# Optimization experiments

Hardware: AMD Instinct MI355X
Metric: run time of the kernel (lower is better)

Reference implementation:

```python
import jax, jax.numpy as jnp
import numpy as np

V, D, H, L, FF, NA, NB, S, C, BS = 32000, 768, 12, 6, 3072, 2, 2, 512, 10, 16
MOE_LAYERS = (1, 3, 5)
NE = NA * NB


def _ln(x, g, b, eps=1e-5):
    m = x.mean(-1, keepdims=True)
    v = ((x - m) ** 2).mean(-1, keepdims=True)
    return (x - m) / jnp.sqrt(v + eps) * g + b


def _ffn(x, W1, B1, W2, B2):
    # GLU-style FFN: w2(a * silu(b)) where [a, b] = chunk(w1(x), 2)
    h = x @ W1.T + B1
    a, b = jnp.split(h, 2, -1)
    return (a * jax.nn.silu(b)) @ W2.T + B2


def _mha(x, wqkv, bqkv, wo, bo):
    Bq, Sq, d = x.shape
    dh = d // H
    qkv = x @ wqkv.T + bqkv
    q, k, v = jnp.split(qkv, 3, -1)
    q = q.reshape(Bq, Sq, H, dh).transpose(0, 2, 1, 3)
    k = k.reshape(Bq, Sq, H, dh).transpose(0, 2, 1, 3)
    v = v.reshape(Bq, Sq, H, dh).transpose(0, 2, 1, 3)
    scores = jnp.einsum('bhqd,bhkd->bhqk', q, k) / jnp.sqrt(jnp.float32(dh))
    attn = jax.nn.softmax(scores, axis=-1)
    o = jnp.einsum('bhqk,bhkd->bhqd', attn, v)
    o = o.transpose(0, 2, 1, 3).reshape(Bq, Sq, d)
    return o @ wo.T + bo


def _moe(xf, W1, B1, W2, B2, gAw, gAb, gBw, gBb):
    pA = jax.nn.softmax(xf @ gAw.T + gAb, axis=-1)  # [T, NA]
    pB = jax.nn.softmax(xf @ gBw.T + gBb, axis=-1)  # [T, NB]
    iA = jnp.argmax(pA, -1)
    iB = jnp.argmax(pB, -1)
    auxA = NA * (pA.mean(0) * jax.nn.one_hot(iA, NA).mean(0)).sum()
    auxB = NB * (pB.mean(0) * jax.nn.one_hot(iB, NB).mean(0)).sum()
    e = iA * NB + iB  # [T] flattened expert id
    # dense all-expert compute then per-token select (E is small = 4)
    h = jnp.einsum('td,efd->etf', xf, W1) + B1[:, None, :]  # [NE, T, 2*FF]
    a, b = jnp.split(h, 2, -1)
    y = jnp.einsum('etf,edf->etd', a * jax.nn.silu(b), W2) + B2[:, None, :]
    out = y[e, jnp.arange(xf.shape[0])]  # [T, D]
    return out, auxA + auxB


def _forward(tok_emb, pos_emb, wqkv, bqkv, wo, bo, ln1g, ln1b, ln2g, ln2b,
             dW1, dB1, dW2, dB2, mW1, mB1, mW2, mB2, gAw, gAb, gBw, gBb,
             cW1, cB1, cW2, cB2, input_ids):
    x = tok_emb[input_ids] + pos_emb[None, :, :]
    total_aux = jnp.float32(0.0)
    di = mi = 0
    for l in range(L):
        x = _ln(x + _mha(x, wqkv[l], bqkv[l], wo[l], bo[l]), ln1g[l], ln1b[l])
        if l in MOE_LAYERS:
            xf = x.reshape(BS * S, D)
            f, aux = _moe(xf, mW1[mi], mB1[mi], mW2[mi], mB2[mi],
                          gAw[mi], gAb[mi], gBw[mi], gBb[mi])
            mi += 1
            total_aux = total_aux + aux
            f = f.reshape(BS, S, D)
        else:
            f = _ffn(x, dW1[di], dB1[di], dW2[di], dB2[di])
            di += 1
        x = _ln(x + f, ln2g[l], ln2b[l])
    rep = x.mean(1)  # mean pooling (no cls token / mask)
    hcls = jax.nn.relu(rep @ cW1.T + cB1)
    logits = hcls @ cW2.T + cB2
    return logits, total_aux


def setup_inputs() -> dict:
    key = jax.random.key(0)
    ks = iter(jax.random.split(key, 48))
    r = lambda shape, s=0.02: jax.random.normal(next(ks), shape, jnp.float32) * s
    Ld, Lm = L - len(MOE_LAYERS), len(MOE_LAYERS)
    return dict(
        input_ids=jax.random.randint(next(ks), (BS, S), 0, V),
        tok_emb=r((V, D)),
        pos_emb=r((S, D), 0.01),
        wqkv=r((L, 3 * D, D)), bqkv=jnp.zeros((L, 3 * D), jnp.float32),
        wo=r((L, D, D)), bo=jnp.zeros((L, D), jnp.float32),
        ln1g=jnp.ones((L, D), jnp.float32), ln1b=jnp.zeros((L, D), jnp.float32),
        ln2g=jnp.ones((L, D), jnp.float32), ln2b=jnp.zeros((L, D), jnp.float32),
        dW1=r((Ld, 2 * FF, D)), dB1=jnp.zeros((Ld, 2 * FF), jnp.float32),
        dW2=r((Ld, D, FF)), dB2=jnp.zeros((Ld, D), jnp.float32),
        mW1=r((Lm, NE, 2 * FF, D)), mB1=jnp.zeros((Lm, NE, 2 * FF), jnp.float32),
        mW2=r((Lm, NE, D, FF)), mB2=jnp.zeros((Lm, NE, D), jnp.float32),
        gAw=r((Lm, NA, D)), gAb=jnp.zeros((Lm, NA), jnp.float32),
        gBw=r((Lm, NB, D)), gBb=jnp.zeros((Lm, NB), jnp.float32),
        cW1=r((D, D)), cB1=jnp.zeros((D,), jnp.float32),
        cW2=r((C, D)), cB2=jnp.zeros((C,), jnp.float32),
    )


def reference(input_ids, tok_emb, pos_emb, wqkv, bqkv, wo, bo, ln1g, ln1b,
              ln2g, ln2b, dW1, dB1, dW2, dB2, mW1, mB1, mW2, mB2,
              gAw, gAb, gBw, gBb, cW1, cB1, cW2, cB2):
    return _forward(tok_emb, pos_emb, wqkv, bqkv, wo, bo, ln1g, ln1b, ln2g,
                    ln2b, dW1, dB1, dW2, dB2, mW1, mB1, mW2, mB2,
                    gAw, gAb, gBw, gBb, cW1, cB1, cW2, cB2, input_ids)
```

## Files before the change

kernel.cpp:

```cpp
#include <hip/hip_runtime.h>
#include <cstddef>

#define TOK   8192
#define DIMD  768
#define NH    12
#define DHD   64
#define SEQ   512
#define NB_   16
#define FFD   3072
#define NEXP  4
#define CCLS  10
#define FF2   (2*FFD)

typedef short bf16x8 __attribute__((ext_vector_type(8)));
typedef float f32x4  __attribute__((ext_vector_type(4)));

static const size_t OFF_X    = 0;
static const size_t OFF_XB   = OFF_X   + (size_t)TOK*DIMD;
static const size_t OFF_F    = OFF_XB  + (size_t)TOK*DIMD/2;
static const size_t OFF_SH   = OFF_F   + (size_t)TOK*DIMD;
static const size_t SH_FL    = (size_t)8704*FF2/2;
static const size_t OFF_WQ   = OFF_SH  + SH_FL;
static const size_t OFF_WOB  = OFF_WQ  + (size_t)3*DIMD*DIMD/2;
static const size_t OFF_W1B  = OFF_WOB + (size_t)DIMD*DIMD/2;
static const size_t OFF_W2B  = OFF_W1B + (size_t)NEXP*FF2*DIMD/2;
static const size_t OFF_REP  = OFF_W2B + (size_t)NEXP*DIMD*FFD/2;
static const size_t OFF_HCLS = OFF_REP + (size_t)NB_*DIMD;
static const size_t OFF_STAT = OFF_HCLS+ (size_t)NB_*DIMD;
static const size_t OFF_INT  = OFF_STAT+ 8;
static const size_t OFF_AUX  = OFF_INT + 160;
static const size_t OFF_EID  = OFF_AUX + 1;
static const size_t OFF_PERM = OFF_EID + TOK;

__device__ __forceinline__ ushort f2bf(float f) {
    union { float f; unsigned u; } v; v.f = f;
    unsigned r = v.u + 0x7FFF + ((v.u >> 16) & 1);
    return (ushort)(r >> 16);
}
__device__ __forceinline__ float bf2f(ushort u) {
    union { unsigned u; float f; } v; v.u = ((unsigned)u) << 16;
    return v.f;
}
__device__ __forceinline__ void gload16(const void* g, void* l) {
    __builtin_amdgcn_global_load_lds((const __attribute__((address_space(1))) void*)g,
                                     (__attribute__((address_space(3))) void*)l, 16, 0, 0);
}

__global__ __launch_bounds__(256) void k_cvt(const float* __restrict__ s, ushort* __restrict__ d, int n8)
{
    int i = blockIdx.x * 256 + threadIdx.x;
    if (i >= n8) return;
    float4 x0 = ((const float4*)s)[i * 2];
    float4 x1 = ((const float4*)s)[i * 2 + 1];
    ushort r[8] = { f2bf(x0.x), f2bf(x0.y), f2bf(x0.z), f2bf(x0.w),
                    f2bf(x1.x), f2bf(x1.y), f2bf(x1.z), f2bf(x1.w) };
    ((uint4*)d)[i] = *(uint4*)r;
}

__global__ __launch_bounds__(256) void k_embed(const int* __restrict__ ids,
                                               const float* __restrict__ te,
                                               const float* __restrict__ pe,
                                               float* __restrict__ x,
                                               ushort* __restrict__ xb)
{
    int i = blockIdx.x * 256 + threadIdx.x;
    const int nd4 = DIMD / 4;
    if (i >= TOK * nd4) return;
    int t = i / nd4, d4 = i % nd4;
    int s = t % SEQ;
    int id = ids[t];
    float4 a = ((const float4*)(te + (size_t)id * DIMD))[d4];
    float4 b = ((const float4*)(pe + (size_t)s  * DIMD))[d4];
    float4 o; o.x = a.x + b.x; o.y = a.y + b.y; o.z = a.z + b.z; o.w = a.w + b.w;
    ((float4*)(x + (size_t)t * DIMD))[d4] = o;
    ushort4 ob = make_ushort4(f2bf(o.x), f2bf(o.y), f2bf(o.z), f2bf(o.w));
    *(ushort4*)(xb + (size_t)t * DIMD + d4 * 4) = ob;
}

template<int GATHER, int SCAT>
__global__ __launch_bounds__(256) void k_mm(const ushort* __restrict__ A,
                                            const ushort* __restrict__ Wb,
                                            const float* __restrict__ bias,
                                            ushort* __restrict__ C_,
                                            int N, int K, int lda,
                                            const int* __restrict__ perm,
                                            const int* __restrict__ offs,
                                            const int* __restrict__ blke,
                                            const int* __restrict__ blkb,
                                            const int* __restrict__ nblk)
{
    constexpr int MOE = GATHER || SCAT;
    __shared__ ushort As[2][4096];
    __shared__ ushort Bs[2][4096];
    __shared__ int    toks[128];
    const int tid = threadIdx.x, lane = tid & 63, w = tid >> 6;
    int bid = blockIdx.y * gridDim.x + blockIdx.x;
    int nwg = gridDim.x * gridDim.y;
    int q = nwg >> 3, r8 = nwg & 7;
    int xcd = bid & 7, loc = bid >> 3;
    int lbid = (xcd < r8 ? xcd * (q + 1) : r8 * (q + 1) + (xcd - r8) * q) + loc;
    const int bx = lbid % gridDim.x, by = lbid / gridDim.x;
    const int n0 = bx * 128, row0 = by * 128;
    const ushort* W = Wb;
    const float*  bi = bias;
    int lb = 0, cnt = 1 << 30;
    if constexpr (MOE) {
        if (by >= *nblk) return;
        int e = blke[by];
        lb = blkb[by];
        int base = offs[e];
        cnt = offs[e + 1] - base;
        W  += (size_t)e * N * K;
        bi += (size_t)e * N;
        if (tid < 128) { int rg = lb + tid; toks[tid] = perm[base + (rg < cnt ? rg : cnt - 1)]; }
        __syncthreads();
    }
    int ar0, ar1;
    if constexpr (GATHER) { ar0 = toks[lane]; ar1 = toks[64 + lane]; }
    else                  { ar0 = row0 + lane; ar1 = row0 + 64 + lane; }
    const ushort* ap0 = A + (size_t)ar0 * lda + w * 8;
    const ushort* ap1 = A + (size_t)ar1 * lda + w * 8;
    const ushort* bp0 = W + (size_t)(n0 + lane) * K + w * 8;
    const ushort* bp1 = W + (size_t)(n0 + 64 + lane) * K + w * 8;

    const int l15 = lane & 15, l4 = lane >> 4;
    const int wm = w >> 1, wn = w & 1;
    f32x4 acc[4][4] = {};

    gload16(ap0, &As[0][w * 1024]);
    gload16(ap1, &As[0][w * 1024 + 512]);
    gload16(bp0, &Bs[0][w * 1024]);
    gload16(bp1, &Bs[0][w * 1024 + 512]);
    __syncthreads();

    const int NT = K / 32;
    int cur = 0;
    for (int t = 0; t < NT; ++t) {
        if (t + 1 < NT) {
            int ko = (t + 1) * 32;
            gload16(ap0 + ko, &As[cur ^ 1][w * 1024]);
            gload16(ap1 + ko, &As[cur ^ 1][w * 1024 + 512]);
            gload16(bp0 + ko, &Bs[cur ^ 1][w * 1024]);
            gload16(bp1 + ko, &Bs[cur ^ 1][w * 1024 + 512]);
        }
        bf16x8 af[4], bf_[4];
#pragma unroll
        for (int i = 0; i < 4; ++i) {
            af[i]  = *(const bf16x8*)&As[cur][l4 * 1024 + (wm * 64 + i * 16 + l15) * 8];
            bf_[i] = *(const bf16x8*)&Bs[cur][l4 * 1024 + (wn * 64 + i * 16 + l15) * 8];
        }
#pragma unroll
        for (int mi = 0; mi < 4; ++mi)
#pragma unroll
            for (int ni = 0; ni < 4; ++ni)
                acc[mi][ni] = __builtin_amdgcn_mfma_f32_16x16x32_bf16(af[mi], bf_[ni], acc[mi][ni], 0, 0, 0);
        __syncthreads();
        cur ^= 1;
    }
#pragma unroll
    for (int ni = 0; ni < 4; ++ni) {
        int col = n0 + wn * 64 + ni * 16 + l15;
        float bb = bi[col];
#pragma unroll
        for (int mi = 0; mi < 4; ++mi) {
            int ri = wm * 64 + mi * 16 + l4 * 4;
#pragma unroll
            for (int r = 0; r < 4; ++r) {
                float o = acc[mi][ni][r] + bb;
                if constexpr (SCAT) {
                    if (lb + ri + r < cnt)
                        C_[(size_t)toks[ri + r] * N + col] = f2bf(o);
                } else {
                    C_[(size_t)(row0 + ri + r) * N + col] = f2bf(o);
                }
            }
        }
    }
}

template<int MOE>
__global__ __launch_bounds__(256) void k_w1g(const ushort* __restrict__ A,
                                             const ushort* __restrict__ Wb,
                                             const float* __restrict__ bias,
                                             ushort* __restrict__ G,
                                             const int* __restrict__ perm,
                                             const int* __restrict__ offs,
                                             const int* __restrict__ blke,
                                             const int* __restrict__ blkb,
                                             const int* __restrict__ nblk)
{
    __shared__ ushort As[2][4096];
    __shared__ ushort Bs[2][8192];
    __shared__ int    toks[128];
    const int tid = threadIdx.x, lane = tid & 63, w = tid >> 6;
    int bid = blockIdx.y * gridDim.x + blockIdx.x;
    int nwg = gridDim.x * gridDim.y;
    int q = nwg >> 3, r8 = nwg & 7;
    int xcd = bid & 7, loc = bid >> 3;
    int lbid = (xcd < r8 ? xcd * (q + 1) : r8 * (q + 1) + (xcd - r8) * q) + loc;
    const int bx = lbid % gridDim.x, by = lbid / gridDim.x;
    const int n0 = bx * 128, row0 = by * 128;
    const ushort* W = Wb;
    const float*  bi = bias;
    if constexpr (MOE) {
        if (by >= *nblk) return;
        int e = blke[by];
        W  += (size_t)e * FF2 * DIMD;
        bi += (size_t)e * FF2;
        int base = offs[e], cnt = offs[e + 1] - base, lb = blkb[by];
        if (tid < 128) { int rg = lb + tid; toks[tid] = perm[base + (rg < cnt ? rg : cnt - 1)]; }
        __syncthreads();
    }
    int ar0, ar1;
    if constexpr (MOE) { ar0 = toks[lane]; ar1 = toks[64 + lane]; }
    else               { ar0 = row0 + lane; ar1 = row0 + 64 + lane; }
    const ushort* ap0  = A + (size_t)ar0 * DIMD + w * 8;
    const ushort* ap1  = A + (size_t)ar1 * DIMD + w * 8;
    const ushort* bpa0 = W + (size_t)(n0 + lane) * DIMD + w * 8;
    const ushort* bpa1 = W + (size_t)(n0 + 64 + lane) * DIMD + w * 8;
    const ushort* bpb0 = W + (size_t)(FFD + n0 + lane) * DIMD + w * 8;
    const ushort* bpb1 = W + (size_t)(FFD + n0 + 64 + lane) * DIMD + w * 8;

    const int l15 = lane & 15, l4 = lane >> 4;
    const int wm = w >> 1, wn = w & 1;
    f32x4 accA[4][4] = {}, accB[4][4] = {};

    gload16(ap0,  &As[0][w * 1024]);
    gload16(ap1,  &As[0][w * 1024 + 512]);
    gload16(bpa0, &Bs[0][w * 2048]);
    gload16(bpa1, &Bs[0][w * 2048 + 512]);
    gload16(bpb0, &Bs[0][w * 2048 + 1024]);
    gload16(bpb1, &Bs[0][w * 2048 + 1536]);
    __syncthreads();

    const int NT = DIMD / 32;
    int cur = 0;
    for (int t = 0; t < NT; ++t) {
        if (t + 1 < NT) {
            int ko = (t + 1) * 32;
            gload16(ap0 + ko,  &As[cur ^ 1][w * 1024]);
            gload16(ap1 + ko,  &As[cur ^ 1][w * 1024 + 512]);
            gload16(bpa0 + ko, &Bs[cur ^ 1][w * 2048]);
            gload16(bpa1 + ko, &Bs[cur ^ 1][w * 2048 + 512]);
            gload16(bpb0 + ko, &Bs[cur ^ 1][w * 2048 + 1024]);
            gload16(bpb1 + ko, &Bs[cur ^ 1][w * 2048 + 1536]);
        }
        bf16x8 af[4], ba[4], bb[4];
#pragma unroll
        for (int i = 0; i < 4; ++i) {
            af[i] = *(const bf16x8*)&As[cur][l4 * 1024 + (wm * 64 + i * 16 + l15) * 8];
            ba[i] = *(const bf16x8*)&Bs[cur][l4 * 2048 + (wn * 64 + i * 16 + l15) * 8];
            bb[i] = *(const bf16x8*)&Bs[cur][l4 * 2048 + 1024 + (wn * 64 + i * 16 + l15) * 8];
        }
#pragma unroll
        for (int mi = 0; mi < 4; ++mi)
#pragma unroll
            for (int ni = 0; ni < 4; ++ni) {
                accA[mi][ni] = __builtin_amdgcn_mfma_f32_16x16x32_bf16(af[mi], ba[ni], accA[mi][ni], 0, 0, 0);
                accB[mi][ni] = __builtin_amdgcn_mfma_f32_16x16x32_bf16(af[mi], bb[ni], accB[mi][ni], 0, 0, 0);
            }
        __syncthreads();
        cur ^= 1;
    }
#pragma unroll
    for (int ni = 0; ni < 4; ++ni) {
        int col = n0 + wn * 64 + ni * 16 + l15;
        float fa = bi[col];
        float fb = bi[FFD + col];
#pragma unroll
        for (int mi = 0; mi < 4; ++mi) {
            int ri = wm * 64 + mi * 16 + l4 * 4;
#pragma unroll
            for (int r = 0; r < 4; ++r) {
                float a = accA[mi][ni][r] + fa;
                float b = accB[mi][ni][r] + fb;
                float g = a * (b / (1.f + __expf(-b)));
                G[(size_t)(row0 + ri + r) * FFD + col] = f2bf(g);
            }
        }
    }
}

__global__ __launch_bounds__(256) void k_attn(const ushort* __restrict__ qkv, ushort* __restrict__ out)
{
    __shared__ ushort Qs[64][72];
    __shared__ ushort Ks[64][72];
    __shared__ ushort Vt[64][72];
    __shared__ ushort Ps[4][16][72];
    const int bh = blockIdx.x;
    const int b = bh / NH, h = bh % NH;
    const int qt = blockIdx.y;
    const int tid = threadIdx.x, lane = tid & 63, w = tid >> 6;
    const int l15 = lane & 15, l4 = lane >> 4;
    const int t0 = b * SEQ + qt * 64;
    {
        int r = tid >> 3, c8 = (tid & 7) * 8;
#pragma unroll
        for (int p = 0; p < 2; ++p) {
            int rr = r + p * 32;
            *(uint4*)&Qs[rr][c8] = *(const uint4*)(qkv + (size_t)(t0 + rr) * 3 * DIMD + h * DHD + c8);
        }
    }
    __syncthreads();
    bf16x8 aq[2];
    aq[0] = *(const bf16x8*)&Qs[w*16 + l15][l4*8];
    aq[1] = *(const bf16x8*)&Qs[w*16 + l15][32 + l4*8];
    f32x4 o[4] = {};
    float m[4], lsum[4];
#pragma unroll
    for (int r = 0; r < 4; ++r) { m[r] = -3.0e38f; lsum[r] = 0.f; }
    for (int kt = 0; kt < SEQ; kt += 64) {
        __syncthreads();
        {
            int r = tid >> 3, c8 = (tid & 7) * 8;
#pragma unroll
            for (int p = 0; p < 2; ++p) {
                int rr = r + p * 32;
                const ushort* kp = qkv + (size_t)(b * SEQ + kt + rr) * 3 * DIMD + DIMD + h * DHD;
                *(uint4*)&Ks[rr][c8] = *(const uint4*)(kp + c8);
                uint4 vv = *(const uint4*)(kp + DIMD + c8);
                const ushort* vs = (const ushort*)&vv;
#pragma unroll
                for (int j = 0; j < 8; ++j) Vt[c8 + j][rr] = vs[j];
            }
        }
        __syncthreads();
        f32x4 s[4] = {};
#pragma unroll
        for (int kk = 0; kk < 2; ++kk)
#pragma unroll
            for (int ni = 0; ni < 4; ++ni) {
                bf16x8 bk = *(const bf16x8*)&Ks[ni*16 + l15][kk*32 + l4*8];
                s[ni] = __builtin_amdgcn_mfma_f32_16x16x32_bf16(aq[kk], bk, s[ni], 0, 0, 0);
            }
        float csc[4];
#pragma unroll
        for (int r = 0; r < 4; ++r) {
            float mx = -3.0e38f;
#pragma unroll
            for (int ni = 0; ni < 4; ++ni) { s[ni][r] *= 0.125f; mx = fmaxf(mx, s[ni][r]); }
            mx = fmaxf(mx, __shfl_xor(mx, 1));
            mx = fmaxf(mx, __shfl_xor(mx, 2));
            mx = fmaxf(mx, __shfl_xor(mx, 4));
            mx = fmaxf(mx, __shfl_xor(mx, 8));
            float nm = fmaxf(m[r], mx);
            float c = __expf(m[r] - nm);
            m[r] = nm;
            float ps = 0.f;
#pragma unroll
            for (int ni = 0; ni < 4; ++ni) { s[ni][r] = __expf(s[ni][r] - nm); ps += s[ni][r]; }
            ps += __shfl_xor(ps, 1);
            ps += __shfl_xor(ps, 2);
            ps += __shfl_xor(ps, 4);
            ps += __shfl_xor(ps, 8);
            lsum[r] = lsum[r] * c + ps;
            csc[r] = c;
#pragma unroll
            for (int ni = 0; ni < 4; ++ni)
                Ps[w][l4*4 + r][ni*16 + l15] = f2bf(s[ni][r]);
        }
#pragma unroll
        for (int di = 0; di < 4; ++di)
#pragma unroll
            for (int r = 0; r < 4; ++r) o[di][r] *= csc[r];
        bf16x8 ap[2];
        ap[0] = *(const bf16x8*)&Ps[w][l15][l4*8];
        ap[1] = *(const bf16x8*)&Ps[w][l15][32 + l4*8];
#pragma unroll
        for (int kk = 0; kk < 2; ++kk)
#pragma unroll
            for (int di = 0; di < 4; ++di) {
                bf16x8 bv = *(const bf16x8*)&Vt[di*16 + l15][kk*32 + l4*8];
                o[di] = __builtin_amdgcn_mfma_f32_16x16x32_bf16(ap[kk], bv, o[di], 0, 0, 0);
            }
    }
    float inv[4];
#pragma unroll
    for (int r = 0; r < 4; ++r) inv[r] = 1.f / lsum[r];
#pragma unroll
    for (int di = 0; di < 4; ++di)
#pragma unroll
        for (int r = 0; r < 4; ++r)
            out[(size_t)(t0 + w*16 + l4*4 + r) * DIMD + h * DHD + di*16 + l15] = f2bf(o[di][r] * inv[r]);
}

__global__ __launch_bounds__(256) void k_ln(float* __restrict__ x, const ushort* __restrict__ fb,
                                            const float* __restrict__ g, const float* __restrict__ b,
                                            ushort* __restrict__ xb)
{
    const int t = blockIdx.x * 4 + (threadIdx.x >> 6);
    const int lane = threadIdx.x & 63;
    float* xr = x + (size_t)t * DIMD;
    const ushort* fr = fb + (size_t)t * DIMD;
    float v[12];
    float s = 0.f, s2 = 0.f;
#pragma unroll
    for (int j = 0; j < 12; ++j) {
        int d = lane + j * 64;
        float val = xr[d] + bf2f(fr[d]);
        v[j] = val; s += val; s2 = fmaf(val, val, s2);
    }
#pragma unroll
    for (int off = 1; off < 64; off <<= 1) {
        s  += __shfl_xor(s,  off);
        s2 += __shfl_xor(s2, off);
    }
    const float mean = s * (1.f / DIMD);
    const float var  = s2 * (1.f / DIMD) - mean * mean;
    const float rstd = rsqrtf(var + 1e-5f);
#pragma unroll
    for (int j = 0; j < 12; ++j) {
        int d = lane + j * 64;
        float o = (v[j] - mean) * rstd * g[d] + b[d];
        xr[d] = o;
        xb[(size_t)t * DIMD + d] = f2bf(o);
    }
}

__global__ __launch_bounds__(256) void k_gate(const float* __restrict__ x,
                                              const float* __restrict__ gAw, const float* __restrict__ gAb,
                                              const float* __restrict__ gBw, const float* __restrict__ gBb,
                                              float* __restrict__ sums, int* __restrict__ cnts,
                                              int* __restrict__ e_id)
{
    const int tid = threadIdx.x, lane = tid & 63, wid = tid >> 6;
    const int gw = blockIdx.x * 4 + wid;
    float wA0[12], wA1[12], wB0[12], wB1[12];
#pragma unroll
    for (int i = 0; i < 12; ++i) {
        int d = lane + i * 64;
        wA0[i] = gAw[d]; wA1[i] = gAw[DIMD + d];
        wB0[i] = gBw[d]; wB1[i] = gBw[DIMD + d];
    }
    const float bA0 = gAb[0], bA1 = gAb[1], bB0 = gBb[0], bB1 = gBb[1];
    float sA0 = 0.f, sA1 = 0.f, sB0 = 0.f, sB1 = 0.f;
    int cA1 = 0, cB1 = 0, cE0 = 0, cE1 = 0, cE2 = 0;
    for (int i = 0; i < 32; ++i) {
        int t = gw * 32 + i;
        const float* xr = x + (size_t)t * DIMD;
        float a0 = 0.f, a1 = 0.f, b0 = 0.f, b1 = 0.f;
#pragma unroll
        for (int j = 0; j < 12; ++j) {
            float v = xr[lane + j * 64];
            a0 = fmaf(v, wA0[j], a0); a1 = fmaf(v, wA1[j], a1);
            b0 = fmaf(v, wB0[j], b0); b1 = fmaf(v, wB1[j], b1);
        }
#pragma unroll
        for (int off = 1; off < 64; off <<= 1) {
            a0 += __shfl_xor(a0, off); a1 += __shfl_xor(a1, off);
            b0 += __shfl_xor(b0, off); b1 += __shfl_xor(b1, off);
        }
        a0 += bA0; a1 += bA1; b0 += bB0; b1 += bB1;
        int iA = (a1 > a0) ? 1 : 0;
        int iB = (b1 > b0) ? 1 : 0;
        float mA = fmaxf(a0, a1); float eA0 = __expf(a0 - mA), eA1 = __expf(a1 - mA);
        float dA = 1.f / (eA0 + eA1);
        float mB = fmaxf(b0, b1); float eB0 = __expf(b0 - mB), eB1 = __expf(b1 - mB);
        float dB = 1.f / (eB0 + eB1);
        sA0 += eA0 * dA; sA1 += eA1 * dA;
        sB0 += eB0 * dB; sB1 += eB1 * dB;
        cA1 += iA; cB1 += iB;
        int e = iA * 2 + iB;
        cE0 += (e == 0); cE1 += (e == 1); cE2 += (e == 2);
        if (lane == 0) e_id[t] = e;
    }
    __shared__ float fpart[4][4];
    __shared__ int   ipart[4][8];
    if (lane == 0) {
        fpart[wid][0] = sA0; fpart[wid][1] = sA1; fpart[wid][2] = sB0; fpart[wid][3] = sB1;
        ipart[wid][0] = 32 - cA1; ipart[wid][1] = cA1;
        ipart[wid][2] = 32 - cB1; ipart[wid][3] = cB1;
        ipart[wid][4] = cE0; ipart[wid][5] = cE1; ipart[wid][6] = cE2;
        ipart[wid][7] = 32 - cE0 - cE1 - cE2;
    }
    __syncthreads();
    if (tid < 4)  atomicAdd(sums + tid, fpart[0][tid] + fpart[1][tid] + fpart[2][tid] + fpart[3][tid]);
    else if (tid >= 64 && tid < 72) {
        int k = tid - 64;
        atomicAdd(cnts + k, ipart[0][k] + ipart[1][k] + ipart[2][k] + ipart[3][k]);
    }
}

__global__ void k_offsets(const int* __restrict__ cntE, int* __restrict__ offs, int* __restrict__ cursor,
                          int* __restrict__ nblk, int* __restrict__ blke, int* __restrict__ blkb)
{
    if (threadIdx.x == 0) {
        int a = 0, nb = 0;
        for (int e = 0; e < NEXP; ++e) {
            offs[e] = a; a += cntE[e]; cursor[e] = 0;
            int blocks = (cntE[e] + 127) >> 7;
            for (int b = 0; b < blocks; ++b) { blke[nb] = e; blkb[nb] = b * 128; ++nb; }
        }
        offs[NEXP] = a;
        *nblk = nb;
    }
}

__global__ __launch_bounds__(256) void k_scatter(const int* __restrict__ e_id, const int* __restrict__ offs,
                                                 int* __restrict__ cursor, int* __restrict__ perm)
{
    int t = blockIdx.x * 256 + threadIdx.x;
    int lane = threadIdx.x & 63;
    int e = e_id[t];
#pragma unroll
    for (int eo = 0; eo < NEXP; ++eo) {
        unsigned long long m = __ballot(e == eo);
        if (m == 0ULL) continue;
        int leader = __ffsll((long long)m) - 1;
        int base = 0;
        if (lane == leader) base = atomicAdd(cursor + eo, (int)__popcll(m));
        base = __shfl(base, leader);
        if (e == eo) {
            int lower = (int)__popcll(m & ((1ULL << lane) - 1ULL));
            perm[offs[eo] + base + lower] = t;
        }
    }
}

__global__ void k_aux(const float* __restrict__ sums, const int* __restrict__ cnts, float* __restrict__ aux_acc)
{
    if (threadIdx.x == 0) {
        const float invT2 = 1.f / ((float)TOK * (float)TOK);
        float aA = 2.f * (sums[0] * (float)cnts[0] + sums[1] * (float)cnts[1]) * invT2;
        float aB = 2.f * (sums[2] * (float)cnts[2] + sums[3] * (float)cnts[3]) * invT2;
        *aux_acc += aA + aB;
    }
}

__global__ __launch_bounds__(256) void k_rep(const float* __restrict__ x, float* __restrict__ rep)
{
    int i = blockIdx.x * 256 + threadIdx.x;
    if (i >= NB_ * DIMD) return;
    int b = i / DIMD, d = i % DIMD;
    float s = 0.f;
    for (int q = 0; q < SEQ; ++q) s += x[((size_t)b * SEQ + q) * DIMD + d];
    rep[i] = s * (1.f / SEQ);
}

__global__ __launch_bounds__(256) void k_cls1(const float* __restrict__ rep, const float* __restrict__ cW1,
                                              const float* __restrict__ cB1, float* __restrict__ hcls)
{
    int w = blockIdx.x * 4 + (threadIdx.x >> 6);
    int lane = threadIdx.x & 63;
    if (w >= NB_ * DIMD) return;
    int b = w / DIMD, i = w % DIMD;
    float s = 0.f;
    for (int d = lane; d < DIMD; d += 64) s += rep[b * DIMD + d] * cW1[(size_t)i * DIMD + d];
    for (int off = 32; off > 0; off >>= 1) s += __shfl_down(s, off);
    if (lane == 0) hcls[w] = fmaxf(s + cB1[i], 0.f);
}

__global__ __launch_bounds__(256) void k_cls2(const float* __restrict__ hcls, const float* __restrict__ cW2,
                                              const float* __restrict__ cB2, float* __restrict__ out)
{
    int w = blockIdx.x * 4 + (threadIdx.x >> 6);
    int lane = threadIdx.x & 63;
    if (w >= NB_ * CCLS) return;
    int b = w / CCLS, c = w % CCLS;
    float s = 0.f;
    for (int d = lane; d < DIMD; d += 64) s += hcls[b * DIMD + d] * cW2[(size_t)c * DIMD + d];
    for (int off = 32; off > 0; off >>= 1) s += __shfl_down(s, off);
    if (lane == 0) out[w] = s + cB2[c];
}

__global__ void k_writeaux(const float* __restrict__ aux_acc, float* __restrict__ out)
{
    if (threadIdx.x == 0) out[NB_ * CCLS] = *aux_acc;
}

extern "C" void kernel_launch(void* const* d_in, const int* in_sizes, int n_in,
                              void* d_out, int out_size, void* d_ws, size_t ws_size,
                              hipStream_t stream)
{
    const int*   input_ids = (const int*)  d_in[0];
    const float* tok_emb   = (const float*)d_in[1];
    const float* pos_emb   = (const float*)d_in[2];
    const float* wqkv      = (const float*)d_in[3];
    const float* bqkv      = (const float*)d_in[4];
    const float* wo        = (const float*)d_in[5];
    const float* bo        = (const float*)d_in[6];
    const float* ln1g      = (const float*)d_in[7];
    const float* ln1b      = (const float*)d_in[8];
    const float* ln2g      = (const float*)d_in[9];
    const float* ln2b      = (const float*)d_in[10];
    const float* dW1       = (const float*)d_in[11];
    const float* dB1       = (const float*)d_in[12];
    const float* dW2       = (const float*)d_in[13];
    const float* dB2       = (const float*)d_in[14];
    const float* mW1       = (const float*)d_in[15];
    const float* mB1       = (const float*)d_in[16];
    const float* mW2       = (const float*)d_in[17];
    const float* mB2       = (const float*)d_in[18];
    const float* gAw       = (const float*)d_in[19];
    const float* gAb       = (const float*)d_in[20];
    const float* gBw       = (const float*)d_in[21];
    const float* gBb       = (const float*)d_in[22];
    const float* cW1       = (const float*)d_in[23];
    const float* cB1       = (const float*)d_in[24];
    const float* cW2       = (const float*)d_in[25];
    const float* cB2       = (const float*)d_in[26];

    float* out = (float*)d_out;
    float* ws  = (float*)d_ws;

    float*  X    = ws + OFF_X;
    ushort* XB   = (ushort*)(ws + OFF_XB);
    ushort* FB   = (ushort*)(ws + OFF_F);
    ushort* QKV  = (ushort*)(ws + OFF_SH);
    ushort* G    = (ushort*)(ws + OFF_SH + (size_t)TOK * 3 * DIMD / 2);
    ushort* Gg   = (ushort*)(ws + OFF_SH);
    ushort* WQB  = (ushort*)(ws + OFF_WQ);
    ushort* WOB  = (ushort*)(ws + OFF_WOB);
    ushort* W1B  = (ushort*)(ws + OFF_W1B);
    ushort* W2B  = (ushort*)(ws + OFF_W2B);
    float*  REP  = ws + OFF_REP;
    float*  HCLS = ws + OFF_HCLS;
    float*  SUMS = ws + OFF_STAT;
    int*    INTB = (int*)(ws + OFF_INT);
    int*    CNTS = INTB;
    int*    OFFS = INTB + 8;
    int*    CURS = INTB + 13;
    int*    NBLK = INTB + 17;
    int*    BLKE = INTB + 18;
    int*    BLKB = INTB + 86;
    float*  AUXP = ws + OFF_AUX;
    int*    EID  = (int*)(ws + OFF_EID);
    int*    PERM = (int*)(ws + OFF_PERM);

    hipMemsetAsync(AUXP, 0, sizeof(float), stream);

    k_embed<<<dim3((TOK * DIMD / 4) / 256), 256, 0, stream>>>(input_ids, tok_emb, pos_emb, X, XB);

    int di = 0, mi = 0;
    for (int l = 0; l < 6; ++l) {
        const int moe = (l == 1 || l == 3 || l == 5);
        {
            int n8 = 3 * DIMD * DIMD / 8;
            k_cvt<<<dim3((n8 + 255) / 256), 256, 0, stream>>>(wqkv + (size_t)l * 3 * DIMD * DIMD, WQB, n8);
            n8 = DIMD * DIMD / 8;
            k_cvt<<<dim3((n8 + 255) / 256), 256, 0, stream>>>(wo + (size_t)l * DIMD * DIMD, WOB, n8);
            if (moe) {
                n8 = NEXP * FF2 * DIMD / 8;
                k_cvt<<<dim3((n8 + 255) / 256), 256, 0, stream>>>(mW1 + (size_t)mi * NEXP * FF2 * DIMD, W1B, n8);
                n8 = NEXP * DIMD * FFD / 8;
                k_cvt<<<dim3((n8 + 255) / 256), 256, 0, stream>>>(mW2 + (size_t)mi * NEXP * DIMD * FFD, W2B, n8);
            } else {
                n8 = FF2 * DIMD / 8;
                k_cvt<<<dim3((n8 + 255) / 256), 256, 0, stream>>>(dW1 + (size_t)di * FF2 * DIMD, W1B, n8);
                n8 = DIMD * FFD / 8;
                k_cvt<<<dim3((n8 + 255) / 256), 256, 0, stream>>>(dW2 + (size_t)di * DIMD * FFD, W2B, n8);
            }
        }
        k_mm<0,0><<<dim3(3 * DIMD / 128, TOK / 128), 256, 0, stream>>>(
            XB, WQB, bqkv + (size_t)l * 3 * DIMD, QKV, 3 * DIMD, DIMD, DIMD,
            nullptr, nullptr, nullptr, nullptr, nullptr);
        k_attn<<<dim3(NB_ * NH, SEQ / 64), 256, 0, stream>>>(QKV, G);
        k_mm<0,0><<<dim3(DIMD / 128, TOK / 128), 256, 0, stream>>>(
            G, WOB, bo + (size_t)l * DIMD, FB, DIMD, DIMD, DIMD,
            nullptr, nullptr, nullptr, nullptr, nullptr);
        k_ln<<<TOK / 4, 256, 0, stream>>>(X, FB, ln1g + (size_t)l * DIMD, ln1b + (size_t)l * DIMD, XB);

        if (moe) {
            hipMemsetAsync(SUMS, 0, 64, stream);
            k_gate<<<64, 256, 0, stream>>>(X,
                gAw + (size_t)mi * 2 * DIMD, gAb + (size_t)mi * 2,
                gBw + (size_t)mi * 2 * DIMD, gBb + (size_t)mi * 2,
                SUMS, CNTS, EID);
            k_offsets<<<1, 1, 0, stream>>>(CNTS + 4, OFFS, CURS, NBLK, BLKE, BLKB);
            k_scatter<<<TOK / 256, 256, 0, stream>>>(EID, OFFS, CURS, PERM);
            k_w1g<1><<<dim3(FFD / 128, 68), 256, 0, stream>>>(
                XB, W1B, mB1 + (size_t)mi * NEXP * FF2, Gg,
                PERM, OFFS, BLKE, BLKB, NBLK);
            k_mm<0,1><<<dim3(DIMD / 128, 68), 256, 0, stream>>>(
                Gg, W2B, mB2 + (size_t)mi * NEXP * DIMD, FB, DIMD, FFD, FFD,
                PERM, OFFS, BLKE, BLKB, NBLK);
            k_aux<<<1, 1, 0, stream>>>(SUMS, CNTS, AUXP);
            ++mi;
        } else {
            k_w1g<0><<<dim3(FFD / 128, TOK / 128), 256, 0, stream>>>(
                XB, W1B, dB1 + (size_t)di * FF2, Gg,
                nullptr, nullptr, nullptr, nullptr, nullptr);
            k_mm<0,0><<<dim3(DIMD / 128, TOK / 128), 256, 0, stream>>>(
                Gg, W2B, dB2 + (size_t)di * DIMD, FB, DIMD, FFD, FFD,
                nullptr, nullptr, nullptr, nullptr, nullptr);
            ++di;
        }
        k_ln<<<TOK / 4, 256, 0, stream>>>(X, FB, ln2g + (size_t)l * DIMD, ln2b + (size_t)l * DIMD, XB);
    }

    k_rep<<<dim3((NB_ * DIMD + 255) / 256), 256, 0, stream>>>(X, REP);
    k_cls1<<<dim3(NB_ * DIMD / 4), 256, 0, stream>>>(REP, cW1, cB1, HCLS);
    k_cls2<<<dim3((NB_ * CCLS + 3) / 4), 256, 0, stream>>>(HCLS, cW2, cB2, out);
    k_writeaux<<<1, 1, 0, stream>>>(AUXP, out);
}
```

Measured before the change: 2.978 ms.

## Triple-buffer GEMM LDS staging with explicit vmcnt waits and one barrier

Changes the k_mm and k_w1g GEMM main loops from double to triple buffering in LDS. Loads are issued two tiles ahead, and raw s_waitcnt vmcnt plus s_barrier replace the two __syncthreads per iteration, so memory latency overlaps more MFMA work with one barrier per step. LDS use grows by half, which may reduce occupancy, and correctness depends on the hand-counted vmcnt values matching the async gload16 count per stage.

```diff
diff --git a/kernel.cpp b/kernel.cpp
--- a/kernel.cpp
+++ b/kernel.cpp
@@ -14,6 +14,9 @@
 
 typedef short bf16x8 __attribute__((ext_vector_type(8)));
 typedef float f32x4  __attribute__((ext_vector_type(4)));
+
+#define ASM_VMCNT(N) asm volatile("s_waitcnt vmcnt(" #N ")" ::: "memory")
+#define ASM_BAR()    asm volatile("s_barrier" ::: "memory")
 
 static const size_t OFF_X    = 0;
 static const size_t OFF_XB   = OFF_X   + (size_t)TOK*DIMD;
@@ -90,8 +93,8 @@
                                             const int* __restrict__ nblk)
 {
     constexpr int MOE = GATHER || SCAT;
-    __shared__ ushort As[2][4096];
-    __shared__ ushort Bs[2][4096];
+    __shared__ ushort As[3][4096];
+    __shared__ ushort Bs[3][4096];
     __shared__ int    toks[128];
     const int tid = threadIdx.x, lane = tid & 63, w = tid >> 6;
     int bid = blockIdx.y * gridDim.x + blockIdx.x;
@@ -127,21 +130,24 @@
     const int wm = w >> 1, wn = w & 1;
     f32x4 acc[4][4] = {};
 
-    gload16(ap0, &As[0][w * 1024]);
-    gload16(ap1, &As[0][w * 1024 + 512]);
-    gload16(bp0, &Bs[0][w * 1024]);
-    gload16(bp1, &Bs[0][w * 1024 + 512]);
-    __syncthreads();
+    auto stage = [&](int t, int buf) {
+        int ko = t * 32;
+        gload16(ap0 + ko, &As[buf][w * 1024]);
+        gload16(ap1 + ko, &As[buf][w * 1024 + 512]);
+        gload16(bp0 + ko, &Bs[buf][w * 1024]);
+        gload16(bp1 + ko, &Bs[buf][w * 1024 + 512]);
+    };
 
     const int NT = K / 32;
+    stage(0, 0);
+    stage(1, 1);
     int cur = 0;
     for (int t = 0; t < NT; ++t) {
-        if (t + 1 < NT) {
-            int ko = (t + 1) * 32;
-            gload16(ap0 + ko, &As[cur ^ 1][w * 1024]);
-            gload16(ap1 + ko, &As[cur ^ 1][w * 1024 + 512]);
-            gload16(bp0 + ko, &Bs[cur ^ 1][w * 1024]);
-            gload16(bp1 + ko, &Bs[cur ^ 1][w * 1024 + 512]);
+        if (t == NT - 1) { ASM_VMCNT(0); } else { ASM_VMCNT(4); }
+        ASM_BAR();
+        if (t + 2 < NT) {
+            int nb = cur + 2; if (nb >= 3) nb -= 3;
+            stage(t + 2, nb);
         }
         bf16x8 af[4], bf_[4];
 #pragma unroll
@@ -154,8 +160,7 @@
 #pragma unroll
             for (int ni = 0; ni < 4; ++ni)
                 acc[mi][ni] = __builtin_amdgcn_mfma_f32_16x16x32_bf16(af[mi], bf_[ni], acc[mi][ni], 0, 0, 0);
-        __syncthreads();
-        cur ^= 1;
+        ++cur; if (cur == 3) cur = 0;
     }
 #pragma unroll
     for (int ni = 0; ni < 4; ++ni) {
@@ -189,8 +194,8 @@
                                              const int* __restrict__ blkb,
                                              const int* __restrict__ nblk)
 {
-    __shared__ ushort As[2][4096];
-    __shared__ ushort Bs[2][8192];
+    __shared__ ushort As[3][4096];
+    __shared__ ushort Bs[3][8192];
     __shared__ int    toks[128];
     const int tid = threadIdx.x, lane = tid & 63, w = tid >> 6;
     int bid = blockIdx.y * gridDim.x + blockIdx.x;
@@ -225,25 +230,26 @@
     const int wm = w >> 1, wn = w & 1;
     f32x4 accA[4][4] = {}, accB[4][4] = {};
 
-    gload16(ap0,  &As[0][w * 1024]);
-    gload16(ap1,  &As[0][w * 1024 + 512]);
-    gload16(bpa0, &Bs[0][w * 2048]);
-    gload16(bpa1, &Bs[0][w * 2048 + 512]);
-    gload16(bpb0, &Bs[0][w * 2048 + 1024]);
-    gload16(bpb1, &Bs[0][w * 2048 + 1536]);
-    __syncthreads();
+    auto stage = [&](int t, int buf) {
+        int ko = t * 32;
+        gload16(ap0 + ko,  &As[buf][w * 1024]);
+        gload16(ap1 + ko,  &As[buf][w * 1024 + 512]);
+        gload16(bpa0 + ko, &Bs[buf][w * 2048]);
+        gload16(bpa1 + ko, &Bs[buf][w * 2048 + 512]);
+        gload16(bpb0 + ko, &Bs[buf][w * 2048 + 1024]);
+        gload16(bpb1 + ko, &Bs[buf][w * 2048 + 1536]);
+    };
 
     const int NT = DIMD / 32;
+    stage(0, 0);
+    stage(1, 1);
     int cur = 0;
     for (int t = 0; t < NT; ++t) {
-        if (t + 1 < NT) {
-            int ko = (t + 1) * 32;
-            gload16(ap0 + ko,  &As[cur ^ 1][w * 1024]);
-            gload16(ap1 + ko,  &As[cur ^ 1][w * 1024 + 512]);
-            gload16(bpa0 + ko, &Bs[cur ^ 1][w * 2048]);
-            gload16(bpa1 + ko, &Bs[cur ^ 1][w * 2048 + 512]);
-            gload16(bpb0 + ko, &Bs[cur ^ 1][w * 2048 + 1024]);
-            gload16(bpb1 + ko, &Bs[cur ^ 1][w * 2048 + 1536]);
+        if (t == NT - 1) { ASM_VMCNT(0); } else { ASM_VMCNT(6); }
+        ASM_BAR();
+        if (t + 2 < NT) {
+            int nb = cur + 2; if (nb >= 3) nb -= 3;
+            stage(t + 2, nb);
         }
         bf16x8 af[4], ba[4], bb[4];
 #pragma unroll
@@ -259,8 +265,7 @@
                 accA[mi][ni] = __builtin_amdgcn_mfma_f32_16x16x32_bf16(af[mi], ba[ni], accA[mi][ni], 0, 0, 0);
                 accB[mi][ni] = __builtin_amdgcn_mfma_f32_16x16x32_bf16(af[mi], bb[ni], accB[mi][ni], 0, 0, 0);
             }
-        __syncthreads();
-        cur ^= 1;
+        ++cur; if (cur == 3) cur = 0;
     }
 #pragma unroll
     for (int ni = 0; ni < 4; ++ni) {
```

Result: slower. 3.669 ms (+23.2%).
